# Optimization experiments

Hardware: AMD Instinct MI355X
Metric: run time of the kernel (lower is better)

The kernel has to match this reference:

```python
import jax, jax.numpy as jnp
import numpy as np

D_IN = 1024
D_OUT = 1024
NUM_HEADS = 16
HEAD_DIM = D_OUT // NUM_HEADS


def setup_inputs() -> dict:
    key = jax.random.key(0)
    ks = jax.random.split(key, 6)
    s = 1.0 / np.sqrt(D_IN)
    return {
        "x": jax.random.normal(ks[0], (4, 2048, D_IN), dtype=jnp.float32),
        "Wq": jax.random.uniform(ks[1], (D_IN, D_OUT), jnp.float32, -s, s),
        "Wk": jax.random.uniform(ks[2], (D_IN, D_OUT), jnp.float32, -s, s),
        "Wv": jax.random.uniform(ks[3], (D_IN, D_OUT), jnp.float32, -s, s),
        "Wo": jax.random.uniform(ks[4], (D_OUT, D_OUT), jnp.float32, -s, s),
        "bo": jax.random.uniform(ks[5], (D_OUT,), jnp.float32, -s, s),
    }


def reference(x, Wq, Wk, Wv, Wo, bo):
    b, n, _ = x.shape
    # QKV projections -> [b, h, n, d]
    def heads(t):
        return t.reshape(b, n, NUM_HEADS, HEAD_DIM).transpose(0, 2, 1, 3)
    q = heads(x @ Wq)
    k = heads(x @ Wk)
    v = heads(x @ Wv)
    # scaled scores with causal mask
    scores = jnp.einsum("bhqd,bhkd->bhqk", q, k) / jnp.sqrt(jnp.float32(HEAD_DIM))
    causal = jnp.tril(jnp.ones((n, n), dtype=bool))  # True = keep
    scores = jnp.where(causal, scores, -jnp.inf)
    attn = jax.nn.softmax(scores, axis=-1)  # dropout p=0.0 -> identity
    ctx = jnp.einsum("bhqk,bhkd->bhqd", attn, v)
    ctx = ctx.transpose(0, 2, 1, 3).reshape(b, n, D_OUT)
    return ctx @ Wo + bo
```

## Files before the change

### kernel.cpp

```cpp
#include <hip/hip_runtime.h>
#include <hip/hip_bf16.h>
#include <math.h>

typedef __attribute__((ext_vector_type(8))) __bf16 bf16x8;
typedef __attribute__((ext_vector_type(4))) __bf16 bf16x4;
typedef __attribute__((ext_vector_type(4))) float f32x4;
typedef __attribute__((ext_vector_type(4))) short short4_t;

#define D_MODEL 1024
#define SEQ     2048
#define BATCH   4
#define NH      16
#define HD      64
#define MROWS   (BATCH * SEQ)

#define SCALE_LOG2E 0.18033688011112042f

__device__ __forceinline__ void gld_lds16(const __bf16* g, __bf16* l) {
  __builtin_amdgcn_global_load_lds(
      (const __attribute__((address_space(1))) void*)g,
      (__attribute__((address_space(3))) void*)l, 16, 0, 0);
}

__global__ __launch_bounds__(256) void cvt_x(const float* __restrict__ in,
                                             __bf16* __restrict__ out) {
  int i = (blockIdx.x * 256 + threadIdx.x) * 4;
  float4 f = *(const float4*)(in + i);
  bf16x4 o;
  o.x = (__bf16)f.x; o.y = (__bf16)f.y; o.z = (__bf16)f.z; o.w = (__bf16)f.w;
  *(bf16x4*)(out + i) = o;
}

__global__ __launch_bounds__(256) void cvt_wt4(const float* __restrict__ W0,
                                               const float* __restrict__ W1,
                                               const float* __restrict__ W2,
                                               const float* __restrict__ W3,
                                               __bf16* __restrict__ Wqkv,
                                               __bf16* __restrict__ Wot) {
  __shared__ __bf16 t[32][33];
  int tx = threadIdx.x, ty = threadIdx.y;
  int z = blockIdx.z;
  const float* W = (z == 0) ? W0 : (z == 1) ? W1 : (z == 2) ? W2 : W3;
  __bf16* Wt = (z < 3) ? (Wqkv + (size_t)z * 1024 * 1024) : Wot;
  int n0 = blockIdx.x * 32, k0 = blockIdx.y * 32;
#pragma unroll
  for (int j = 0; j < 32; j += 8)
    t[ty + j][tx] = (__bf16)W[(size_t)(k0 + ty + j) * D_MODEL + n0 + tx];
  __syncthreads();
#pragma unroll
  for (int j = 0; j < 32; j += 8)
    Wt[(size_t)(n0 + ty + j) * D_MODEL + k0 + tx] = t[tx][ty + j];
}

template <int EPI>
__global__ __launch_bounds__(256) void gemm_bt(const __bf16* __restrict__ A,
                                               const __bf16* __restrict__ Bt,
                                               const float* __restrict__ bias,
                                               void* __restrict__ Cout) {
  constexpr int Kd = 1024;
  constexpr bool SWAP = (EPI != 1);
  __shared__ __bf16 As[128 * 32];
  __shared__ __bf16 Bs[128 * 32];
  const int tid = threadIdx.x;
  const int lane = tid & 63;
  const int w = tid >> 6;
  const int quad = lane >> 4, l16 = lane & 15;
  const int wr = w >> 1, wc = w & 1;
  const int tm = blockIdx.y * 128, tn = blockIdx.x * 128;

  f32x4 acc[4][4] = {};

  const int u0 = (w * 2) * 64 + lane;
  const int u1 = u0 + 64;
  const int rA0 = u0 >> 2, kofs0 = (u0 & 3) * 8;
  const int rA1 = u1 >> 2, kofs1 = (u1 & 3) * 8;
  const __bf16* gA0 = A + (size_t)(tm + rA0) * Kd + kofs0;
  const __bf16* gA1 = A + (size_t)(tm + rA1) * Kd + kofs1;
  const __bf16* gB0 = Bt + (size_t)(tn + rA0) * Kd + kofs0;
  const __bf16* gB1 = Bt + (size_t)(tn + rA1) * Kd + kofs1;
  __bf16* lA0 = As + (w * 2 + 0) * 512;
  __bf16* lA1 = As + (w * 2 + 1) * 512;
  __bf16* lB0 = Bs + (w * 2 + 0) * 512;
  __bf16* lB1 = Bs + (w * 2 + 1) * 512;

  for (int k0 = 0; k0 < Kd; k0 += 32) {
    gld_lds16(gA0 + k0, lA0);
    gld_lds16(gA1 + k0, lA1);
    gld_lds16(gB0 + k0, lB0);
    gld_lds16(gB1 + k0, lB1);
    __syncthreads();
    bf16x8 af[4], bfr[4];
#pragma unroll
    for (int t = 0; t < 4; ++t) {
      af[t]  = *(const bf16x8*)&As[(wr * 64 + t * 16 + l16) * 32 + quad * 8];
      bfr[t] = *(const bf16x8*)&Bs[(wc * 64 + t * 16 + l16) * 32 + quad * 8];
    }
#pragma unroll
    for (int mt = 0; mt < 4; ++mt)
#pragma unroll
      for (int nt = 0; nt < 4; ++nt) {
        if constexpr (SWAP)
          acc[mt][nt] = __builtin_amdgcn_mfma_f32_16x16x32_bf16(
              bfr[nt], af[mt], acc[mt][nt], 0, 0, 0);
        else
          acc[mt][nt] = __builtin_amdgcn_mfma_f32_16x16x32_bf16(
              af[mt], bfr[nt], acc[mt][nt], 0, 0, 0);
      }
    __syncthreads();
  }

#pragma unroll
  for (int mt = 0; mt < 4; ++mt)
#pragma unroll
    for (int nt = 0; nt < 4; ++nt) {
      if constexpr (EPI == 2) {
        int gm  = tm + wr * 64 + mt * 16 + l16;
        int gn0 = tn + wc * 64 + nt * 16 + quad * 4;
        float4 bv = *(const float4*)&bias[gn0];
        float4 o;
        o.x = acc[mt][nt][0] + bv.x;
        o.y = acc[mt][nt][1] + bv.y;
        o.z = acc[mt][nt][2] + bv.z;
        o.w = acc[mt][nt][3] + bv.w;
        *(float4*)&((float*)Cout)[(size_t)gm * 1024 + gn0] = o;
      } else if constexpr (EPI == 0) {
        int gm = tm + wr * 64 + mt * 16 + l16;
        int f0 = tn + wc * 64 + nt * 16 + quad * 4;
        int which = f0 >> 10, col = f0 & 1023;
        int b = gm >> 11, nn = gm & 2047, h = col >> 6, d = col & 63;
        float s = (which == 0) ? SCALE_LOG2E : 1.0f;
        bf16x4 o;
        o[0] = (__bf16)(acc[mt][nt][0] * s);
        o[1] = (__bf16)(acc[mt][nt][1] * s);
        o[2] = (__bf16)(acc[mt][nt][2] * s);
        o[3] = (__bf16)(acc[mt][nt][3] * s);
        __bf16* op = (__bf16*)Cout + (size_t)which * (BATCH * SEQ * (size_t)D_MODEL) +
                     ((size_t)(b * NH + h) * SEQ + nn) * HD + d;
        *(bf16x4*)op = o;
      } else {
        int gm0 = tm + wr * 64 + mt * 16 + quad * 4;
        int gn  = tn + wc * 64 + nt * 16 + l16;
        int b = gm0 >> 11, nn0 = gm0 & 2047, h = gn >> 6, d = gn & 63;
        bf16x4 o;
        o[0] = (__bf16)acc[mt][nt][0];
        o[1] = (__bf16)acc[mt][nt][1];
        o[2] = (__bf16)acc[mt][nt][2];
        o[3] = (__bf16)acc[mt][nt][3];
        __bf16* op = (__bf16*)Cout + ((size_t)(b * NH + h) * HD + d) * SEQ + nn0;
        *(bf16x4*)op = o;
      }
    }
}

__global__ __launch_bounds__(256, 2) void attn(const __bf16* __restrict__ Q,
                                               const __bf16* __restrict__ K,
                                               const __bf16* __restrict__ Vt,
                                               __bf16* __restrict__ ctx) {
  const int tid = threadIdx.x;
  const int lane = tid & 63, w = tid >> 6;
  const int quad = lane >> 4, l16 = lane & 15;
  const int byy = blockIdx.y;
  const int pr = (byy < 4) ? byy : 11 - byy;
  const int bh = blockIdx.x;
  const int tile0 = pr, tile1 = 15 - pr;
  const __bf16* qb = Q + (size_t)bh * SEQ * HD;
  const __bf16* kb = K + (size_t)bh * SEQ * HD;
  const __bf16* vb = Vt + (size_t)bh * HD * SEQ;

  __shared__ __bf16 KsAll[2 * 4096];
  __shared__ __bf16 VsAll[2 * 4096];

  const int qmin[2] = {tile0 * 128 + w * 32, tile1 * 128 + w * 32};

  bf16x8 aq[2][2][2];
#pragma unroll
  for (int p = 0; p < 2; ++p)
#pragma unroll
    for (int qq = 0; qq < 2; ++qq)
#pragma unroll
      for (int kk = 0; kk < 2; ++kk)
        aq[p][qq][kk] = *(const bf16x8*)(qb + (size_t)(qmin[p] + qq * 16 + l16) * HD +
                                         kk * 32 + quad * 8);

  f32x4 acc[2][2][4] = {};
  float lsum[2][2] = {};

  const int u0 = w * 128 + lane;
  const int u1 = u0 + 64;
  const int kOffG0 = ((u0 >> 2) & 63) * HD + (u0 >> 8) * 32 + (u0 & 3) * 8;
  const int kOffG1 = ((u1 >> 2) & 63) * HD + (u1 >> 8) * 32 + (u1 & 3) * 8;
  const int vd0 = u0 >> 3, vd1 = u1 >> 3;
  const int vOffG0 = vd0 * SEQ + (((u0 & 7) ^ (vd0 & 7)) * 8);
  const int vOffG1 = vd1 * SEQ + (((u1 & 7) ^ (vd1 & 7)) * 8);

  auto stage = [&](int k0s, int bufsel) {
    __bf16* Kb = KsAll + bufsel * 4096;
    __bf16* Vb = VsAll + bufsel * 4096;
    gld_lds16(kb + (size_t)k0s * HD + kOffG0, Kb + u0 * 8);
    gld_lds16(kb + (size_t)k0s * HD + kOffG1, Kb + u1 * 8);
    gld_lds16(vb + k0s + vOffG0, Vb + u0 * 8);
    gld_lds16(vb + k0s + vOffG1, Vb + u1 * 8);
  };

  const int nIter = 2 * tile1 + 2;
  stage(0, 0);

  for (int it = 0; it < nIter; ++it) {
    __syncthreads();
    if (it + 1 < nIter) stage((it + 1) * 64, (it + 1) & 1);

    const int k0 = it * 64;
    if (k0 <= qmin[1] + 31) {
      const __bf16* Kb = KsAll + (it & 1) * 4096;
      const __bf16* Vb = VsAll + (it & 1) * 4096;

      bf16x8 bk[4][2];
#pragma unroll
      for (int kt = 0; kt < 4; ++kt)
#pragma unroll
        for (int kk = 0; kk < 2; ++kk)
          bk[kt][kk] = *(const bf16x8*)&Kb[kk * 2048 + (kt * 16 + l16) * 32 + quad * 8];

      short4_t vf[4][4];
#pragma unroll
      for (int kt = 0; kt < 4; ++kt)
#pragma unroll
        for (int cd = 0; cd < 4; ++cd)
          vf[kt][cd] = *(const short4_t*)&Vb[(cd * 16 + l16) * 64 +
                                             (((kt * 2 + (quad >> 1)) ^ (l16 & 7)) * 8) +
                                             (quad & 1) * 4];

#pragma unroll
      for (int p = 0; p < 2; ++p) {
        if (k0 > qmin[p] + 31) continue;
        f32x4 St[4][2] = {};
#pragma unroll
        for (int kt = 0; kt < 4; ++kt)
#pragma unroll
          for (int qq = 0; qq < 2; ++qq) {
            St[kt][qq] = __builtin_amdgcn_mfma_f32_16x16x32_bf16(
                bk[kt][0], aq[p][qq][0], St[kt][qq], 0, 0, 0);
            St[kt][qq] = __builtin_amdgcn_mfma_f32_16x16x32_bf16(
                bk[kt][1], aq[p][qq][1], St[kt][qq], 0, 0, 0);
          }
        const bool full = (k0 + 63 <= qmin[p]);
#pragma unroll
        for (int kt = 0; kt < 4; ++kt)
#pragma unroll
          for (int qq = 0; qq < 2; ++qq) {
            float e0 = __builtin_amdgcn_exp2f(St[kt][qq][0]);
            float e1 = __builtin_amdgcn_exp2f(St[kt][qq][1]);
            float e2 = __builtin_amdgcn_exp2f(St[kt][qq][2]);
            float e3 = __builtin_amdgcn_exp2f(St[kt][qq][3]);
            if (!full) {
              int kg = k0 + kt * 16 + quad * 4;
              int qg = qmin[p] + qq * 16 + l16;
              if (kg + 0 > qg) e0 = 0.f;
              if (kg + 1 > qg) e1 = 0.f;
              if (kg + 2 > qg) e2 = 0.f;
              if (kg + 3 > qg) e3 = 0.f;
            }
            lsum[p][qq] += (e0 + e1) + (e2 + e3);
            short4_t ap;
            ap[0] = __builtin_bit_cast(short, (__bf16)e0);
            ap[1] = __builtin_bit_cast(short, (__bf16)e1);
            ap[2] = __builtin_bit_cast(short, (__bf16)e2);
            ap[3] = __builtin_bit_cast(short, (__bf16)e3);
#pragma unroll
            for (int cd = 0; cd < 4; ++cd)
              acc[p][qq][cd] = __builtin_amdgcn_mfma_f32_16x16x16bf16_1k(
                  ap, vf[kt][cd], acc[p][qq][cd], 0, 0, 0);
          }
      }
    }
  }

  const int bb = bh >> 4, hh = bh & 15;
#pragma unroll
  for (int p = 0; p < 2; ++p) {
#pragma unroll
    for (int qq = 0; qq < 2; ++qq) {
      float s = lsum[p][qq];
      s += __shfl_xor(s, 16);
      s += __shfl_xor(s, 32);
      float rinv[4];
#pragma unroll
      for (int i = 0; i < 4; ++i)
        rinv[i] = 1.0f / __shfl(s, (lane & 48) + quad * 4 + i);
#pragma unroll
      for (int c = 0; c < 4; ++c)
#pragma unroll
        for (int i = 0; i < 4; ++i) {
          int q = qmin[p] + qq * 16 + quad * 4 + i;
          float o = acc[p][qq][c][i] * rinv[i];
          ctx[((size_t)(bb * SEQ + q)) * D_MODEL + hh * HD + c * 16 + l16] = (__bf16)o;
        }
    }
  }
}

extern "C" void kernel_launch(void* const* d_in, const int* in_sizes, int n_in,
                              void* d_out, int out_size, void* d_ws, size_t ws_size,
                              hipStream_t stream) {
  const float* x  = (const float*)d_in[0];
  const float* Wq = (const float*)d_in[1];
  const float* Wk = (const float*)d_in[2];
  const float* Wv = (const float*)d_in[3];
  const float* Wo = (const float*)d_in[4];
  const float* bo = (const float*)d_in[5];
  float* out = (float*)d_out;
  char* ws = (char*)d_ws;
  const size_t MB = 1024 * 1024;
  __bf16* xb   = (__bf16*)(ws);
  __bf16* Wqkv = (__bf16*)(ws + 16 * MB);
  __bf16* Wot  = (__bf16*)(ws + 22 * MB);
  __bf16* Qh   = (__bf16*)(ws + 24 * MB);
  __bf16* Kh   = (__bf16*)(ws + 40 * MB);
  __bf16* Vth  = (__bf16*)(ws + 56 * MB);
  __bf16* ctx  = xb;

  cvt_x<<<MROWS * D_MODEL / (256 * 4), 256, 0, stream>>>(x, xb);
  cvt_wt4<<<dim3(32, 32, 4), dim3(32, 8), 0, stream>>>(Wq, Wk, Wv, Wo, Wqkv, Wot);

  gemm_bt<0><<<dim3(16, 64), 256, 0, stream>>>(xb, Wqkv, nullptr, Qh);
  gemm_bt<1><<<dim3(8, 64), 256, 0, stream>>>(xb, Wqkv + 2 * 1024 * 1024, nullptr, Vth);

  attn<<<dim3(64, 8), 256, 0, stream>>>(Qh, Kh, Vth, ctx);

  gemm_bt<2><<<dim3(8, 64), 256, 0, stream>>>(ctx, Wot, bo, out);
}
```

Measured before the change: 263.8 us.

## Split paired causal query tiles into separate attention blocks with higher occupancy

The attention kernel previously had each block process two query tiles (a short and a long one, for causal load balance) and share the K/V staging between them. Now each block handles a single 128-row query tile. The grid doubles to 1024 blocks, launch bounds allow 4 blocks per CU, and the tile order interleaves short and long tiles. This reduces registers per thread and raises parallelism. In exchange, K/V tiles are loaded from global memory more often because the two tiles no longer share staging, and per-block work becomes imbalanced.

```diff
diff --git a/kernel.cpp b/kernel.cpp
--- a/kernel.cpp
+++ b/kernel.cpp
@@ -152,7 +152,7 @@
     }
 }
 
-__global__ __launch_bounds__(256, 2) void attn(const __bf16* __restrict__ Q,
+__global__ __launch_bounds__(256, 4) void attn(const __bf16* __restrict__ Q,
                                                const __bf16* __restrict__ K,
                                                const __bf16* __restrict__ Vt,
                                                __bf16* __restrict__ ctx) {
@@ -160,9 +160,8 @@
   const int lane = tid & 63, w = tid >> 6;
   const int quad = lane >> 4, l16 = lane & 15;
   const int byy = blockIdx.y;
-  const int pr = (byy < 4) ? byy : 11 - byy;
+  const int tile = (byy & 1) ? (15 - (byy >> 1)) : (byy >> 1);
   const int bh = blockIdx.x;
-  const int tile0 = pr, tile1 = 15 - pr;
   const __bf16* qb = Q + (size_t)bh * SEQ * HD;
   const __bf16* kb = K + (size_t)bh * SEQ * HD;
   const __bf16* vb = Vt + (size_t)bh * HD * SEQ;
@@ -170,20 +169,18 @@
   __shared__ __bf16 KsAll[2 * 4096];
   __shared__ __bf16 VsAll[2 * 4096];
 
-  const int qmin[2] = {tile0 * 128 + w * 32, tile1 * 128 + w * 32};
-
-  bf16x8 aq[2][2][2];
-#pragma unroll
-  for (int p = 0; p < 2; ++p)
-#pragma unroll
-    for (int qq = 0; qq < 2; ++qq)
-#pragma unroll
-      for (int kk = 0; kk < 2; ++kk)
-        aq[p][qq][kk] = *(const bf16x8*)(qb + (size_t)(qmin[p] + qq * 16 + l16) * HD +
-                                         kk * 32 + quad * 8);
-
-  f32x4 acc[2][2][4] = {};
-  float lsum[2][2] = {};
+  const int qmin = tile * 128 + w * 32;
+
+  bf16x8 aq[2][2];
+#pragma unroll
+  for (int qq = 0; qq < 2; ++qq)
+#pragma unroll
+    for (int kk = 0; kk < 2; ++kk)
+      aq[qq][kk] = *(const bf16x8*)(qb + (size_t)(qmin + qq * 16 + l16) * HD +
+                                    kk * 32 + quad * 8);
+
+  f32x4 acc[2][4] = {};
+  float lsum[2] = {};
 
   const int u0 = w * 128 + lane;
   const int u1 = u0 + 64;
@@ -202,7 +199,7 @@
     gld_lds16(vb + k0s + vOffG1, Vb + u1 * 8);
   };
 
-  const int nIter = 2 * tile1 + 2;
+  const int nIter = 2 * tile + 2;
   stage(0, 0);
 
   for (int it = 0; it < nIter; ++it) {
@@ -210,7 +207,7 @@
     if (it + 1 < nIter) stage((it + 1) * 64, (it + 1) & 1);
 
     const int k0 = it * 64;
-    if (k0 <= qmin[1] + 31) {
+    if (k0 <= qmin + 31) {
       const __bf16* Kb = KsAll + (it & 1) * 4096;
       const __bf16* Vb = VsAll + (it & 1) * 4096;
 
@@ -230,72 +227,65 @@
                                              (((kt * 2 + (quad >> 1)) ^ (l16 & 7)) * 8) +
                                              (quad & 1) * 4];
 
-#pragma unroll
-      for (int p = 0; p < 2; ++p) {
-        if (k0 > qmin[p] + 31) continue;
-        f32x4 St[4][2] = {};
-#pragma unroll
-        for (int kt = 0; kt < 4; ++kt)
-#pragma unroll
-          for (int qq = 0; qq < 2; ++qq) {
-            St[kt][qq] = __builtin_amdgcn_mfma_f32_16x16x32_bf16(
-                bk[kt][0], aq[p][qq][0], St[kt][qq], 0, 0, 0);
-            St[kt][qq] = __builtin_amdgcn_mfma_f32_16x16x32_bf16(
-                bk[kt][1], aq[p][qq][1], St[kt][qq], 0, 0, 0);
+      f32x4 St[4][2] = {};
+#pragma unroll
+      for (int kt = 0; kt < 4; ++kt)
+#pragma unroll
+        for (int qq = 0; qq < 2; ++qq) {
+          St[kt][qq] = __builtin_amdgcn_mfma_f32_16x16x32_bf16(
+              bk[kt][0], aq[qq][0], St[kt][qq], 0, 0, 0);
+          St[kt][qq] = __builtin_amdgcn_mfma_f32_16x16x32_bf16(
+              bk[kt][1], aq[qq][1], St[kt][qq], 0, 0, 0);
+        }
+      const bool full = (k0 + 63 <= qmin);
+#pragma unroll
+      for (int kt = 0; kt < 4; ++kt)
+#pragma unroll
+        for (int qq = 0; qq < 2; ++qq) {
+          float e0 = __builtin_amdgcn_exp2f(St[kt][qq][0]);
+          float e1 = __builtin_amdgcn_exp2f(St[kt][qq][1]);
+          float e2 = __builtin_amdgcn_exp2f(St[kt][qq][2]);
+          float e3 = __builtin_amdgcn_exp2f(St[kt][qq][3]);
+          if (!full) {
+            int kg = k0 + kt * 16 + quad * 4;
+            int qg = qmin + qq * 16 + l16;
+            if (kg + 0 > qg) e0 = 0.f;
+            if (kg + 1 > qg) e1 = 0.f;
+            if (kg + 2 > qg) e2 = 0.f;
+            if (kg + 3 > qg) e3 = 0.f;
           }
-        const bool full = (k0 + 63 <= qmin[p]);
-#pragma unroll
-        for (int kt = 0; kt < 4; ++kt)
-#pragma unroll
-          for (int qq = 0; qq < 2; ++qq) {
-            float e0 = __builtin_amdgcn_exp2f(St[kt][qq][0]);
-            float e1 = __builtin_amdgcn_exp2f(St[kt][qq][1]);
-            float e2 = __builtin_amdgcn_exp2f(St[kt][qq][2]);
-            float e3 = __builtin_amdgcn_exp2f(St[kt][qq][3]);
-            if (!full) {
-              int kg = k0 + kt * 16 + quad * 4;
-              int qg = qmin[p] + qq * 16 + l16;
-              if (kg + 0 > qg) e0 = 0.f;
-              if (kg + 1 > qg) e1 = 0.f;
-              if (kg + 2 > qg) e2 = 0.f;
-              if (kg + 3 > qg) e3 = 0.f;
-            }
-            lsum[p][qq] += (e0 + e1) + (e2 + e3);
-            short4_t ap;
-            ap[0] = __builtin_bit_cast(short, (__bf16)e0);
-            ap[1] = __builtin_bit_cast(short, (__bf16)e1);
-            ap[2] = __builtin_bit_cast(short, (__bf16)e2);
-            ap[3] = __builtin_bit_cast(short, (__bf16)e3);
-#pragma unroll
-            for (int cd = 0; cd < 4; ++cd)
-              acc[p][qq][cd] = __builtin_amdgcn_mfma_f32_16x16x16bf16_1k(
-                  ap, vf[kt][cd], acc[p][qq][cd], 0, 0, 0);
-          }
-      }
+          lsum[qq] += (e0 + e1) + (e2 + e3);
+          short4_t ap;
+          ap[0] = __builtin_bit_cast(short, (__bf16)e0);
+          ap[1] = __builtin_bit_cast(short, (__bf16)e1);
+          ap[2] = __builtin_bit_cast(short, (__bf16)e2);
+          ap[3] = __builtin_bit_cast(short, (__bf16)e3);
+#pragma unroll
+          for (int cd = 0; cd < 4; ++cd)
+            acc[qq][cd] = __builtin_amdgcn_mfma_f32_16x16x16bf16_1k(
+                ap, vf[kt][cd], acc[qq][cd], 0, 0, 0);
+        }
     }
   }
 
   const int bb = bh >> 4, hh = bh & 15;
 #pragma unroll
-  for (int p = 0; p < 2; ++p) {
-#pragma unroll
-    for (int qq = 0; qq < 2; ++qq) {
-      float s = lsum[p][qq];
-      s += __shfl_xor(s, 16);
-      s += __shfl_xor(s, 32);
-      float rinv[4];
-#pragma unroll
-      for (int i = 0; i < 4; ++i)
-        rinv[i] = 1.0f / __shfl(s, (lane & 48) + quad * 4 + i);
-#pragma unroll
-      for (int c = 0; c < 4; ++c)
-#pragma unroll
-        for (int i = 0; i < 4; ++i) {
-          int q = qmin[p] + qq * 16 + quad * 4 + i;
-          float o = acc[p][qq][c][i] * rinv[i];
-          ctx[((size_t)(bb * SEQ + q)) * D_MODEL + hh * HD + c * 16 + l16] = (__bf16)o;
-        }
-    }
+  for (int qq = 0; qq < 2; ++qq) {
+    float s = lsum[qq];
+    s += __shfl_xor(s, 16);
+    s += __shfl_xor(s, 32);
+    float rinv[4];
+#pragma unroll
+    for (int i = 0; i < 4; ++i)
+      rinv[i] = 1.0f / __shfl(s, (lane & 48) + quad * 4 + i);
+#pragma unroll
+    for (int c = 0; c < 4; ++c)
+#pragma unroll
+      for (int i = 0; i < 4; ++i) {
+        int q = qmin + qq * 16 + quad * 4 + i;
+        float o = acc[qq][c][i] * rinv[i];
+        ctx[((size_t)(bb * SEQ + q)) * D_MODEL + hh * HD + c * 16 + l16] = (__bf16)o;
+      }
   }
 }
 
@@ -325,7 +315,7 @@
   gemm_bt<0><<<dim3(16, 64), 256, 0, stream>>>(xb, Wqkv, nullptr, Qh);
   gemm_bt<1><<<dim3(8, 64), 256, 0, stream>>>(xb, Wqkv + 2 * 1024 * 1024, nullptr, Vth);
 
-  attn<<<dim3(64, 8), 256, 0, stream>>>(Qh, Kh, Vth, ctx);
+  attn<<<dim3(64, 16), 256, 0, stream>>>(Qh, Kh, Vth, ctx);
 
   gemm_bt<2><<<dim3(8, 64), 256, 0, stream>>>(ctx, Wot, bo, out);
 }
```

Result: slower. 307.3 us (+16.5%).
